# Kernel tuning notes

Hardware: AMD Instinct MI355X
Metric: run time of the kernel (lower is better)

The kernel has to match this reference:

```python
import jax, jax.numpy as jnp
import numpy as np

B, CIN, COUT, H, W = 4, 256, 128, 64, 64

def conv1x1(x, w, b):
    # x: [B,C,H,W], w: [O,C], b: [O]
    return jnp.einsum('bchw,oc->bohw', x, w) + b[None, :, None, None]

def setup_inputs() -> dict:
    key = jax.random.key(0)
    ks = jax.random.split(key, 9)
    s_in = 1.0 / np.sqrt(CIN)
    s_out = 1.0 / np.sqrt(COUT)
    return {
        'x': jax.random.normal(ks[0], (B, CIN, H, W), dtype=jnp.float32),
        'w_theta': jax.random.normal(ks[1], (COUT, CIN), dtype=jnp.float32) * s_in,
        'b_theta': jax.random.normal(ks[2], (COUT,), dtype=jnp.float32) * s_in,
        'w_phi': jax.random.normal(ks[3], (COUT, CIN), dtype=jnp.float32) * s_in,
        'b_phi': jax.random.normal(ks[4], (COUT,), dtype=jnp.float32) * s_in,
        'w_g': jax.random.normal(ks[5], (COUT, CIN), dtype=jnp.float32) * s_in,
        'b_g': jax.random.normal(ks[6], (COUT,), dtype=jnp.float32) * s_in,
        'w_W': jax.random.normal(ks[7], (CIN, COUT), dtype=jnp.float32) * s_out,
        'b_W': jax.random.normal(ks[8], (CIN,), dtype=jnp.float32) * s_out,
    }

def reference(x, w_theta, b_theta, w_phi, b_phi, w_g, b_g, w_W, b_W):
    b, c, h, w = x.shape
    n = h * w
    co = w_theta.shape[0]
    theta_x = conv1x1(x, w_theta, b_theta).reshape(b, co, n).transpose(0, 2, 1)  # [B,N,Co]
    phi_x = conv1x1(x, w_phi, b_phi).reshape(b, co, n)                            # [B,Co,N]
    g_x = conv1x1(x, w_g, b_g).reshape(b, co, n).transpose(0, 2, 1)               # [B,N,Co]
    scores = jnp.einsum('bnc,bcm->bnm', theta_x, phi_x)                           # [B,N,N]
    attn = jax.nn.softmax(scores, axis=-1)
    y = jnp.einsum('bnm,bmc->bnc', attn, g_x)                                     # [B,N,Co]
    y = y.transpose(0, 2, 1).reshape(b, co, h, w)
    z = conv1x1(y, w_W, b_W) + x
    return z
```

## Files before the change

### kernel.cpp

```cpp
#include <hip/hip_runtime.h>

#define B_    4
#define C_    256
#define O_    128
#define N_    4096
#define THW   256
#define TILES 64

typedef __attribute__((ext_vector_type(8))) _Float16 f16x8;
typedef __attribute__((ext_vector_type(4))) float    f32x4;

struct __align__(8) us4 { unsigned short x, y, z, w; };

__device__ __forceinline__ float bf2f(unsigned short u) {
    unsigned v = ((unsigned)u) << 16;
    union { unsigned u; float f; } c; c.u = v; return c.f;
}
__device__ __forceinline__ unsigned short f2bf(float f) {
    union { float f; unsigned u; } c; c.f = f;
    unsigned r = c.u + 0x7fffu + ((c.u >> 16) & 1u);
    return (unsigned short)(r >> 16);
}
__device__ __forceinline__ unsigned short f2h(float f) {
    _Float16 h = (_Float16)f;
    union { _Float16 h; unsigned short s; } c; c.h = h; return c.s;
}
__device__ __forceinline__ float h2f(unsigned short s) {
    union { unsigned short s; _Float16 h; } c; c.s = s; return (float)c.h;
}

__device__ __forceinline__ void load4f(const void* base, size_t idx, int isf32, float o[4]) {
    if (isf32) {
        float4 v = *(const float4*)((const float*)base + idx);
        o[0] = v.x; o[1] = v.y; o[2] = v.z; o[3] = v.w;
    } else {
        us4 v = *(const us4*)((const unsigned short*)base + idx);
        o[0] = bf2f(v.x); o[1] = bf2f(v.y); o[2] = bf2f(v.z); o[3] = bf2f(v.w);
    }
}
__device__ __forceinline__ float load1f(const void* base, size_t idx, int isf32) {
    return isf32 ? ((const float*)base)[idx] : bf2f(((const unsigned short*)base)[idx]);
}

__global__ __launch_bounds__(256) void detect_kernel(
    const unsigned short* __restrict__ xu, int* __restrict__ flag)
{
    __shared__ int cnt;
    if (threadIdx.x == 0) cnt = 0;
    __syncthreads();
    int local = 0;
    for (int i = threadIdx.x; i < 4096; i += 256) {
        unsigned short u = xu[2 * i];
        int e = (u >> 7) & 0xFF;
        if (e == 0xFF || e >= 0x90 || (e > 0 && e <= 0x60)) local++;
    }
    atomicAdd(&cnt, local);
    __syncthreads();
    if (threadIdx.x == 0) *flag = (cnt > 1024) ? 1 : 0;
}

__global__ __launch_bounds__(256) void qkv_kernel(
    const void* __restrict__ x,
    const void* __restrict__ wt, const void* __restrict__ wp,
    const void* __restrict__ wg,
    const void* __restrict__ bt, const void* __restrict__ bp,
    const void* __restrict__ bg,
    const int*  __restrict__ flag,
    unsigned short* __restrict__ thph,
    unsigned short* __restrict__ gT)
{
    const int isf32 = *flag;
    const int jsel = blockIdx.y;
    const void* w  = jsel == 0 ? wt : (jsel == 1 ? wp : wg);
    const void* bi = jsel == 0 ? bt : (jsel == 1 ? bp : bg);
    const int b  = blockIdx.z;
    const int n0 = blockIdx.x * 64;
    const int tid  = threadIdx.x;
    const int wv   = tid >> 6, lane = tid & 63;
    const int quad = lane >> 4, l16 = lane & 15;

    __shared__ alignas(16) unsigned short smem[64 * 72 + 128 * 72];
    unsigned short (*As)[72] = (unsigned short(*)[72])smem;
    unsigned short (*Bs)[72] = (unsigned short(*)[72])(smem + 64 * 72);

    f32x4 acc[8];
    for (int i = 0; i < 8; i++) acc[i] = (f32x4)0.f;

    for (int kc = 0; kc < C_; kc += 64) {
        __syncthreads();
        for (int it = 0; it < 4; it++) {
            int l = it * 256 + tid;
            int c = l >> 4;
            int ng = l & 15;
            float v[4];
            load4f(x, (size_t)(b * C_ + kc + c) * N_ + n0 + ng * 4, isf32, v);
            int g = c >> 3, cl = c & 7;
            int swz = ((g ^ (ng & 7)) << 3) + cl;
            As[ng * 4 + 0][swz] = f2h(v[0]);
            As[ng * 4 + 1][swz] = f2h(v[1]);
            As[ng * 4 + 2][swz] = f2h(v[2]);
            As[ng * 4 + 3][swz] = f2h(v[3]);
        }
        for (int it = 0; it < 8; it++) {
            int l = it * 256 + tid;
            int j = l >> 4;
            int cg = l & 15;
            float v[4];
            load4f(w, (size_t)j * C_ + kc + cg * 4, isf32, v);
            Bs[j][cg * 4 + 0] = f2h(v[0]);
            Bs[j][cg * 4 + 1] = f2h(v[1]);
            Bs[j][cg * 4 + 2] = f2h(v[2]);
            Bs[j][cg * 4 + 3] = f2h(v[3]);
        }
        __syncthreads();
        for (int s = 0; s < 2; s++) {
            int row = wv * 16 + l16;
            int g2 = ((s * 4 + quad) ^ ((row >> 2) & 7)) << 3;
            f16x8 a = *(const f16x8*)&As[row][g2];
            for (int jt = 0; jt < 8; jt++) {
                f16x8 bb = *(const f16x8*)&Bs[jt * 16 + l16][s * 32 + quad * 8];
                acc[jt] = __builtin_amdgcn_mfma_f32_16x16x32_f16(a, bb, acc[jt], 0, 0, 0);
            }
        }
    }

    if (jsel < 2) {
        for (int jt = 0; jt < 8; jt++) {
            int j = jt * 16 + l16;
            float bias = load1f(bi, j, isf32);
            for (int r = 0; r < 4; r++) {
                int n = n0 + wv * 16 + quad * 4 + r;
                thph[(size_t)(b * N_ + n) * THW + jsel * O_ + j] = f2h(acc[jt][r] + bias);
            }
        }
    } else {
        unsigned short (*T)[68] = (unsigned short(*)[68])smem;
        __syncthreads();
        for (int jt = 0; jt < 8; jt++) {
            int j = jt * 16 + l16;
            float bias = load1f(bi, j, isf32);
            for (int r = 0; r < 4; r++) {
                int nl = wv * 16 + quad * 4 + r;
                T[j][nl] = f2h(acc[jt][r] + bias);
            }
        }
        __syncthreads();
        for (int it = 0; it < 8; it++) {
            int l = it * 256 + tid;
            int j = l >> 4;
            int ng = l & 15;
            *(us4*)(gT + ((size_t)(b * O_ + j)) * N_ + n0 + ng * 4) = *(const us4*)&T[j][ng * 4];
        }
    }
}

__global__ __launch_bounds__(256, 2) void attn_partial(
    const unsigned short* __restrict__ thph,
    const unsigned short* __restrict__ gT,
    unsigned short* __restrict__ partO,
    float* __restrict__ pm,
    float* __restrict__ pl,
    int S)
{
    const int b    = blockIdx.z;
    const int s_id = blockIdx.y;
    const int n0   = blockIdx.x * 128;
    const int tid  = threadIdx.x;
    const int wv   = tid >> 6, lane = tid & 63;
    const int quad = lane >> 4, l16 = lane & 15;

    const int t0 = (TILES * s_id) / S;
    const int t1 = (TILES * (s_id + 1)) / S;

    __shared__ alignas(16) unsigned short Ks[64][136];
    __shared__ alignas(16) unsigned short Gs[128][72];
    __shared__ alignas(16) unsigned short Ps[4][32][72];

    const int wq0 = n0 + wv * 32;

    f16x8 qf[2][4];
    #pragma unroll
    for (int qg = 0; qg < 2; qg++) {
        const unsigned short* qp = thph + (size_t)(b * N_ + wq0 + qg * 16 + l16) * THW;
        #pragma unroll
        for (int s = 0; s < 4; s++)
            qf[qg][s] = *(const f16x8*)(qp + s * 32 + quad * 8);
    }

    f32x4 oacc[2][8];
    #pragma unroll
    for (int qg = 0; qg < 2; qg++)
        #pragma unroll
        for (int i = 0; i < 8; i++) oacc[qg][i] = (f32x4)0.f;
    float mst[2] = { -INFINITY, -INFINITY };
    float lst[2] = { 0.f, 0.f };

    const int krow = tid >> 4, kog = tid & 15;
    const int grow = tid >> 3, gng = tid & 7;
    const unsigned short* kb_g = thph + (size_t)(b * N_ + krow) * THW + O_ + kog * 8;
    const unsigned short* gb_g = gT + ((size_t)(b * O_ + grow)) * N_ + gng * 8;

    f16x8 kreg[4], greg[4];
    auto prefetch = [&](int mt) {
        int m0 = mt * 64;
        #pragma unroll
        for (int it = 0; it < 4; it++)
            kreg[it] = *(const f16x8*)(kb_g + (size_t)(m0 + it * 16) * THW);
        #pragma unroll
        for (int it = 0; it < 4; it++)
            greg[it] = *(const f16x8*)(gb_g + m0 + (size_t)it * 32 * N_);
    };
    prefetch(t0);

    for (int mt = t0; mt < t1; mt++) {
        __syncthreads();
        #pragma unroll
        for (int it = 0; it < 4; it++)
            *(f16x8*)&Ks[krow + it * 16][kog * 8] = kreg[it];
        #pragma unroll
        for (int it = 0; it < 4; it++)
            *(f16x8*)&Gs[grow + it * 32][gng * 8] = greg[it];
        __syncthreads();
        if (mt + 1 < t1) prefetch(mt + 1);

        f32x4 sacc[2][4];
        #pragma unroll
        for (int qg = 0; qg < 2; qg++)
            #pragma unroll
            for (int kt = 0; kt < 4; kt++) sacc[qg][kt] = (f32x4)0.f;
        #pragma unroll
        for (int s = 0; s < 4; s++) {
            #pragma unroll
            for (int kt = 0; kt < 4; kt++) {
                f16x8 kb = *(const f16x8*)&Ks[kt * 16 + l16][s * 32 + quad * 8];
                sacc[0][kt] = __builtin_amdgcn_mfma_f32_16x16x32_f16(kb, qf[0][s], sacc[0][kt], 0, 0, 0);
                sacc[1][kt] = __builtin_amdgcn_mfma_f32_16x16x32_f16(kb, qf[1][s], sacc[1][kt], 0, 0, 0);
            }
        }

        #pragma unroll
        for (int qg = 0; qg < 2; qg++) {
            float rm = fmaxf(
                fmaxf(fmaxf(fmaxf(sacc[qg][0][0], sacc[qg][0][1]), fmaxf(sacc[qg][0][2], sacc[qg][0][3])),
                      fmaxf(fmaxf(sacc[qg][1][0], sacc[qg][1][1]), fmaxf(sacc[qg][1][2], sacc[qg][1][3]))),
                fmaxf(fmaxf(fmaxf(sacc[qg][2][0], sacc[qg][2][1]), fmaxf(sacc[qg][2][2], sacc[qg][2][3])),
                      fmaxf(fmaxf(sacc[qg][3][0], sacc[qg][3][1]), fmaxf(sacc[qg][3][2], sacc[qg][3][3]))));
            rm = fmaxf(rm, __shfl_xor(rm, 16));
            rm = fmaxf(rm, __shfl_xor(rm, 32));

            float mnew  = fmaxf(mst[qg], rm);
            float alpha = __expf(mst[qg] - mnew);
            mst[qg] = mnew;

            float rs = 0.f;
            unsigned short* prow = &Ps[wv][qg * 16 + l16][quad * 4];
            #pragma unroll
            for (int kt = 0; kt < 4; kt++) {
                float p0 = __expf(sacc[qg][kt][0] - mnew);
                float p1 = __expf(sacc[qg][kt][1] - mnew);
                float p2 = __expf(sacc[qg][kt][2] - mnew);
                float p3 = __expf(sacc[qg][kt][3] - mnew);
                rs += (p0 + p1) + (p2 + p3);
                us4 pk;
                pk.x = f2h(p0); pk.y = f2h(p1); pk.z = f2h(p2); pk.w = f2h(p3);
                *(us4*)(prow + kt * 16) = pk;
            }
            rs += __shfl_xor(rs, 16);
            rs += __shfl_xor(rs, 32);
            lst[qg] = lst[qg] * alpha + rs;

            #pragma unroll
            for (int jt = 0; jt < 8; jt++) oacc[qg][jt] *= alpha;
        }

        #pragma unroll
        for (int s = 0; s < 2; s++) {
            f16x8 pb0 = *(const f16x8*)&Ps[wv][l16][s * 32 + quad * 8];
            f16x8 pb1 = *(const f16x8*)&Ps[wv][16 + l16][s * 32 + quad * 8];
            #pragma unroll
            for (int jt = 0; jt < 8; jt++) {
                f16x8 ga = *(const f16x8*)&Gs[jt * 16 + l16][s * 32 + quad * 8];
                oacc[0][jt] = __builtin_amdgcn_mfma_f32_16x16x32_f16(ga, pb0, oacc[0][jt], 0, 0, 0);
                oacc[1][jt] = __builtin_amdgcn_mfma_f32_16x16x32_f16(ga, pb1, oacc[1][jt], 0, 0, 0);
            }
        }
    }

    #pragma unroll
    for (int qg = 0; qg < 2; qg++) {
        int n = wq0 + qg * 16 + l16;
        size_t rowb = ((size_t)(s_id * B_ + b) * N_ + n) * O_;
        #pragma unroll
        for (int jt = 0; jt < 8; jt++) {
            us4 v;
            v.x = f2h(oacc[qg][jt][0]);
            v.y = f2h(oacc[qg][jt][1]);
            v.z = f2h(oacc[qg][jt][2]);
            v.w = f2h(oacc[qg][jt][3]);
            *(us4*)(partO + rowb + jt * 16 + quad * 4) = v;
        }
        if (quad == 0) {
            pm[(size_t)(s_id * B_ + b) * N_ + n] = mst[qg];
            pl[(size_t)(s_id * B_ + b) * N_ + n] = lst[qg];
        }
    }
}

__global__ __launch_bounds__(256) void merge_kernel(
    const unsigned short* __restrict__ partO,
    const float* __restrict__ pm, const float* __restrict__ pl,
    unsigned short* __restrict__ y,
    int S)
{
    int idx = blockIdx.x * 256 + threadIdx.x;
    int bn  = idx >> 5;
    int og  = idx & 31;
    const int BN = B_ * N_;

    float M = -INFINITY;
    for (int s = 0; s < S; s++) M = fmaxf(M, pm[(size_t)s * BN + bn]);
    float w[4];
    float L = 0.f;
    for (int s = 0; s < S; s++) {
        w[s] = __expf(pm[(size_t)s * BN + bn] - M);
        L += w[s] * pl[(size_t)s * BN + bn];
    }
    float inv = 1.0f / L;

    float a0 = 0.f, a1 = 0.f, a2 = 0.f, a3 = 0.f;
    for (int s = 0; s < S; s++) {
        us4 v = *(const us4*)(partO + ((size_t)s * BN + bn) * O_ + og * 4);
        a0 += h2f(v.x) * w[s];
        a1 += h2f(v.y) * w[s];
        a2 += h2f(v.z) * w[s];
        a3 += h2f(v.w) * w[s];
    }
    us4 r;
    r.x = f2h(a0 * inv); r.y = f2h(a1 * inv);
    r.z = f2h(a2 * inv); r.w = f2h(a3 * inv);
    *(us4*)(y + (size_t)bn * O_ + og * 4) = r;
}

__global__ __launch_bounds__(256) void out_kernel(
    const unsigned short* __restrict__ y,
    const void* __restrict__ wW,
    const void* __restrict__ bW,
    const void* __restrict__ x,
    const int*  __restrict__ flag,
    void* __restrict__ z)
{
    const int isf32 = *flag;
    const int b  = blockIdx.z;
    const int c0 = blockIdx.y * 64;
    const int n0 = blockIdx.x * 128;
    const int tid  = threadIdx.x;
    const int wv   = tid >> 6, lane = tid & 63;
    const int quad = lane >> 4, l16 = lane & 15;

    __shared__ alignas(16) unsigned short Ys[128][136];
    __shared__ alignas(16) unsigned short Ws[64][136];

    for (int it = 0; it < 16; it++) {
        int l = it * 256 + tid;
        int nn = l >> 5;
        int og = l & 31;
        us4 v = *(const us4*)(y + (size_t)(b * N_ + n0 + nn) * O_ + og * 4);
        *(us4*)&Ys[nn][og * 4] = v;
    }
    for (int it = 0; it < 8; it++) {
        int l = it * 256 + tid;
        int cc = l >> 5;
        int og = l & 31;
        float v[4];
        load4f(wW, (size_t)(c0 + cc) * O_ + og * 4, isf32, v);
        Ws[cc][og * 4 + 0] = f2h(v[0]);
        Ws[cc][og * 4 + 1] = f2h(v[1]);
        Ws[cc][og * 4 + 2] = f2h(v[2]);
        Ws[cc][og * 4 + 3] = f2h(v[3]);
    }
    __syncthreads();

    f32x4 acc[8];
    for (int i = 0; i < 8; i++) acc[i] = (f32x4)0.f;
    for (int s = 0; s < 4; s++) {
        f16x8 a = *(const f16x8*)&Ws[wv * 16 + l16][s * 32 + quad * 8];
        for (int nt = 0; nt < 8; nt++) {
            f16x8 bb = *(const f16x8*)&Ys[nt * 16 + l16][s * 32 + quad * 8];
            acc[nt] = __builtin_amdgcn_mfma_f32_16x16x32_f16(a, bb, acc[nt], 0, 0, 0);
        }
    }
    for (int r = 0; r < 4; r++) {
        int c = c0 + wv * 16 + quad * 4 + r;
        float bias = load1f(bW, c, isf32);
        for (int nt = 0; nt < 8; nt++) {
            int n = n0 + nt * 16 + l16;
            size_t idx = (size_t)(b * C_ + c) * N_ + n;
            float zv = acc[nt][r] + bias + load1f(x, idx, isf32);
            if (isf32) ((float*)z)[idx] = zv;
            else       ((unsigned short*)z)[idx] = f2bf(zv);
        }
    }
}

extern "C" void kernel_launch(void* const* d_in, const int* in_sizes, int n_in,
                              void* d_out, int out_size, void* d_ws, size_t ws_size,
                              hipStream_t stream) {
    const void* x  = d_in[0];
    const void* wt = d_in[1];
    const void* bt = d_in[2];
    const void* wp = d_in[3];
    const void* bp = d_in[4];
    const void* wg = d_in[5];
    const void* bg = d_in[6];
    const void* wW = d_in[7];
    const void* bW = d_in[8];

    const size_t base = 64 + 8388608  + 4194304 ;
    const size_t per_split = 4194304  + 131072 ;
    int S = 4;
    while (S > 1 && base + (size_t)S * per_split > ws_size) S--;

    char* p = (char*)d_ws;
    int* flag = (int*)p;                    p += 64;
    unsigned short* thph = (unsigned short*)p;  p += 8388608;
    unsigned short* gT   = (unsigned short*)p;  p += 4194304;
    unsigned short* partO = (unsigned short*)p; p += (size_t)S * 4194304;
    float* pm = (float*)p;                  p += (size_t)S * 65536;
    float* pl = (float*)p;
    unsigned short* y = gT;

    detect_kernel<<<1, 256, 0, stream>>>((const unsigned short*)x, flag);

    dim3 g1(N_ / 64, 3, B_);
    qkv_kernel<<<g1, 256, 0, stream>>>(x, wt, wp, wg, bt, bp, bg, flag, thph, gT);

    dim3 g2(N_ / 128, S, B_);
    attn_partial<<<g2, 256, 0, stream>>>(thph, gT, partO, pm, pl, S);

    merge_kernel<<<(B_ * N_ * 32) / 256, 256, 0, stream>>>(partO, pm, pl, y, S);

    dim3 g3(N_ / 128, C_ / 64, B_);
    out_kernel<<<g3, 256, 0, stream>>>(y, wW, bW, x, flag, d_out);
}
```

Before: 182.2 us.

## Use exp2 softmax with lazy rescaling, setprio around MFMAs, raise occupancy and splits

Folds log2(e) into theta at projection time so the softmax can use exp2f, and skips the running-max rescale of the accumulators unless the max grows by more than 8. Brackets the MFMA blocks with s_setprio, raises attn_partial's launch bounds to 3 blocks per CU, and raises the split count from 4 to 6, which the merge loop now handles without a fixed-size array. Also packs the shared-memory weight stores into 8-byte writes. The lazy rescale lets fp16 probabilities reach up to 2^8, which risks some precision loss, and the higher occupancy target may cause register spills.

```diff
diff --git a/kernel.cpp b/kernel.cpp
--- a/kernel.cpp
+++ b/kernel.cpp
@@ -107,10 +107,9 @@
             int cg = l & 15;
             float v[4];
             load4f(w, (size_t)j * C_ + kc + cg * 4, isf32, v);
-            Bs[j][cg * 4 + 0] = f2h(v[0]);
-            Bs[j][cg * 4 + 1] = f2h(v[1]);
-            Bs[j][cg * 4 + 2] = f2h(v[2]);
-            Bs[j][cg * 4 + 3] = f2h(v[3]);
+            us4 pk;
+            pk.x = f2h(v[0]); pk.y = f2h(v[1]); pk.z = f2h(v[2]); pk.w = f2h(v[3]);
+            *(us4*)&Bs[j][cg * 4] = pk;
         }
         __syncthreads();
         for (int s = 0; s < 2; s++) {
@@ -125,12 +124,13 @@
     }
 
     if (jsel < 2) {
+        const float scale = (jsel == 0) ? 1.44269504f : 1.0f;
         for (int jt = 0; jt < 8; jt++) {
             int j = jt * 16 + l16;
             float bias = load1f(bi, j, isf32);
             for (int r = 0; r < 4; r++) {
                 int n = n0 + wv * 16 + quad * 4 + r;
-                thph[(size_t)(b * N_ + n) * THW + jsel * O_ + j] = f2h(acc[jt][r] + bias);
+                thph[(size_t)(b * N_ + n) * THW + jsel * O_ + j] = f2h((acc[jt][r] + bias) * scale);
             }
         }
     } else {
@@ -154,7 +154,7 @@
     }
 }
 
-__global__ __launch_bounds__(256, 2) void attn_partial(
+__global__ __launch_bounds__(256, 3) void attn_partial(
     const unsigned short* __restrict__ thph,
     const unsigned short* __restrict__ gT,
     unsigned short* __restrict__ partO,
@@ -228,6 +228,7 @@
         for (int qg = 0; qg < 2; qg++)
             #pragma unroll
             for (int kt = 0; kt < 4; kt++) sacc[qg][kt] = (f32x4)0.f;
+        __builtin_amdgcn_s_setprio(1);
         #pragma unroll
         for (int s = 0; s < 4; s++) {
             #pragma unroll
@@ -237,6 +238,7 @@
                 sacc[1][kt] = __builtin_amdgcn_mfma_f32_16x16x32_f16(kb, qf[1][s], sacc[1][kt], 0, 0, 0);
             }
         }
+        __builtin_amdgcn_s_setprio(0);
 
         #pragma unroll
         for (int qg = 0; qg < 2; qg++) {
@@ -248,18 +250,24 @@
             rm = fmaxf(rm, __shfl_xor(rm, 16));
             rm = fmaxf(rm, __shfl_xor(rm, 32));
 
-            float mnew  = fmaxf(mst[qg], rm);
-            float alpha = __expf(mst[qg] - mnew);
-            mst[qg] = mnew;
+            if (__any(rm > mst[qg] + 8.0f)) {
+                float mnew  = fmaxf(mst[qg], rm);
+                float alpha = exp2f(mst[qg] - mnew);
+                mst[qg] = mnew;
+                lst[qg] *= alpha;
+                #pragma unroll
+                for (int jt = 0; jt < 8; jt++) oacc[qg][jt] *= alpha;
+            }
+            const float m = mst[qg];
 
             float rs = 0.f;
             unsigned short* prow = &Ps[wv][qg * 16 + l16][quad * 4];
             #pragma unroll
             for (int kt = 0; kt < 4; kt++) {
-                float p0 = __expf(sacc[qg][kt][0] - mnew);
-                float p1 = __expf(sacc[qg][kt][1] - mnew);
-                float p2 = __expf(sacc[qg][kt][2] - mnew);
-                float p3 = __expf(sacc[qg][kt][3] - mnew);
+                float p0 = exp2f(sacc[qg][kt][0] - m);
+                float p1 = exp2f(sacc[qg][kt][1] - m);
+                float p2 = exp2f(sacc[qg][kt][2] - m);
+                float p3 = exp2f(sacc[qg][kt][3] - m);
                 rs += (p0 + p1) + (p2 + p3);
                 us4 pk;
                 pk.x = f2h(p0); pk.y = f2h(p1); pk.z = f2h(p2); pk.w = f2h(p3);
@@ -267,12 +275,10 @@
             }
             rs += __shfl_xor(rs, 16);
             rs += __shfl_xor(rs, 32);
-            lst[qg] = lst[qg] * alpha + rs;
-
-            #pragma unroll
-            for (int jt = 0; jt < 8; jt++) oacc[qg][jt] *= alpha;
-        }
-
+            lst[qg] += rs;
+        }
+
+        __builtin_amdgcn_s_setprio(1);
         #pragma unroll
         for (int s = 0; s < 2; s++) {
             f16x8 pb0 = *(const f16x8*)&Ps[wv][l16][s * 32 + quad * 8];
@@ -284,6 +290,7 @@
                 oacc[1][jt] = __builtin_amdgcn_mfma_f32_16x16x32_f16(ga, pb1, oacc[1][jt], 0, 0, 0);
             }
         }
+        __builtin_amdgcn_s_setprio(0);
     }
 
     #pragma unroll
@@ -319,22 +326,20 @@
 
     float M = -INFINITY;
     for (int s = 0; s < S; s++) M = fmaxf(M, pm[(size_t)s * BN + bn]);
-    float w[4];
+
     float L = 0.f;
-    for (int s = 0; s < S; s++) {
-        w[s] = __expf(pm[(size_t)s * BN + bn] - M);
-        L += w[s] * pl[(size_t)s * BN + bn];
-    }
-    float inv = 1.0f / L;
-
     float a0 = 0.f, a1 = 0.f, a2 = 0.f, a3 = 0.f;
     for (int s = 0; s < S; s++) {
+        float ws = exp2f(pm[(size_t)s * BN + bn] - M);
+        L += ws * pl[(size_t)s * BN + bn];
         us4 v = *(const us4*)(partO + ((size_t)s * BN + bn) * O_ + og * 4);
-        a0 += h2f(v.x) * w[s];
-        a1 += h2f(v.y) * w[s];
-        a2 += h2f(v.z) * w[s];
-        a3 += h2f(v.w) * w[s];
-    }
+        a0 += h2f(v.x) * ws;
+        a1 += h2f(v.y) * ws;
+        a2 += h2f(v.z) * ws;
+        a3 += h2f(v.w) * ws;
+    }
+    float inv = 1.0f / L;
+
     us4 r;
     r.x = f2h(a0 * inv); r.y = f2h(a1 * inv);
     r.z = f2h(a2 * inv); r.w = f2h(a3 * inv);
@@ -373,10 +378,9 @@
         int og = l & 31;
         float v[4];
         load4f(wW, (size_t)(c0 + cc) * O_ + og * 4, isf32, v);
-        Ws[cc][og * 4 + 0] = f2h(v[0]);
-        Ws[cc][og * 4 + 1] = f2h(v[1]);
-        Ws[cc][og * 4 + 2] = f2h(v[2]);
-        Ws[cc][og * 4 + 3] = f2h(v[3]);
+        us4 pk;
+        pk.x = f2h(v[0]); pk.y = f2h(v[1]); pk.z = f2h(v[2]); pk.w = f2h(v[3]);
+        *(us4*)&Ws[cc][og * 4] = pk;
     }
     __syncthreads();
 
@@ -417,7 +421,7 @@
 
     const size_t base = 64 + 8388608  + 4194304 ;
     const size_t per_split = 4194304  + 131072 ;
-    int S = 4;
+    int S = 6;
     while (S > 1 && base + (size_t)S * per_split > ws_size) S--;
 
     char* p = (char*)d_ws;
```

After: 263.7 us. 1.45x slower.
